# Kernel optimization log

Measured on AMD Instinct MI355X. Metric: run time of the kernel, lower is better.

The kernel has to match this reference:

```python
import jax, jax.numpy as jnp
import numpy as np


def _maxpool2x2(x):
    # x: [N, C, H, W] -> [N, C, H//2, W//2]
    N, C, H, W = x.shape
    x = x.reshape(N, C, H // 2, 2, W // 2, 2)
    return x.max(axis=(3, 5))


def setup_inputs() -> dict:
    key = jax.random.key(0)
    ks = jax.random.split(key, 6)
    N, C, H, W = 16, 64, 64, 64
    x = jax.random.normal(ks[0], (N, C, H, W), dtype=jnp.float32)
    # 1x1 conv weights, stored as [out_ch, in_ch] (kernel is 1x1, no bias)
    w_theta = jax.random.normal(ks[1], (C >> 3, C), dtype=jnp.float32) * 0.05
    w_phi = jax.random.normal(ks[2], (C >> 3, C), dtype=jnp.float32) * 0.05
    w_g = jax.random.normal(ks[3], (C >> 1, C), dtype=jnp.float32) * 0.05
    w_o = jax.random.normal(ks[4], (C, C >> 1), dtype=jnp.float32) * 0.05
    gamma = jax.random.normal(ks[5], (), dtype=jnp.float32)
    return {"x": x, "w_theta": w_theta, "w_phi": w_phi, "w_g": w_g, "w_o": w_o, "gamma": gamma}


def reference(x, w_theta, w_phi, w_g, w_o, gamma):
    N, C, H, W = x.shape
    L = H * W           # location_num
    D = L >> 2          # downsampled_num
    # 1x1 convs as channel contractions
    theta = jnp.einsum('oc,nchw->nohw', w_theta, x).reshape(N, C >> 3, L)
    phi = _maxpool2x2(jnp.einsum('oc,nchw->nohw', w_phi, x)).reshape(N, C >> 3, D)
    attn = jax.nn.softmax(jnp.einsum('nkl,nkd->nld', theta, phi), axis=-1)  # [N, L, D]
    g = _maxpool2x2(jnp.einsum('oc,nchw->nohw', w_g, x)).reshape(N, C >> 1, D)
    attn_g = jnp.einsum('ngd,nld->ngl', g, attn).reshape(N, C >> 1, H, W)
    attn_g = jnp.einsum('og,nghw->nohw', w_o, attn_g)
    return x + gamma * attn_g
```

## Files before the change

### kernel.cpp

```cpp
#include <hip/hip_runtime.h>
#include <hip/hip_bf16.h>
#include <hip/hip_fp16.h>

#define NB 16
#define CCH 64
#define LL 4096
#define DD 1024

typedef _Float16 h8 __attribute__((ext_vector_type(8)));
typedef _Float16 h2 __attribute__((ext_vector_type(2)));
typedef float    f4v __attribute__((ext_vector_type(4)));

#if defined(__has_builtin)
#if __has_builtin(__builtin_amdgcn_fdot2)
#define HAVE_FDOT2 1
#endif
#if __has_builtin(__builtin_amdgcn_exp2f)
#define EXP2F(x) __builtin_amdgcn_exp2f(x)
#endif
#endif
#ifndef EXP2F
#define EXP2F(x) exp2f(x)
#endif

static __device__ __forceinline__ float fdot2f(h2 a, h2 b, float c) {
#ifdef HAVE_FDOT2
    return __builtin_amdgcn_fdot2(a, b, c, false);
#else
    return c + (float)a[0] * (float)b[0] + (float)a[1] * (float)b[1];
#endif
}

#define MFMA16(a, b, c) __builtin_amdgcn_mfma_f32_16x16x32_f16((a), (b), (c), 0, 0, 0)

__global__ __launch_bounds__(256) void prep_kernel(
    const float* __restrict__ x,
    const float* __restrict__ w_theta,
    const float* __restrict__ w_phi,
    const float* __restrict__ w_g,
    _Float16* __restrict__ theta_out,
    _Float16* __restrict__ phi_out,
    _Float16* __restrict__ gT_out)
{
    __shared__ float part[64][193];

    const int n    = blockIdx.x >> 6;
    const int rem  = blockIdx.x & 63;
    const int rg   = rem >> 1;
    const int half = rem & 1;
    const int tid  = threadIdx.x;
    const int cs   = tid >> 6;
    const int pix  = tid & 63;
    const int row  = pix >> 5;
    const int col  = pix & 31;
    const int l    = (rg * 2 + row) * 64 + half * 32 + col;

    const float* xp = x + (size_t)n * CCH * LL + l;
    float xv[16];
#pragma unroll
    for (int c = 0; c < 16; ++c) xv[c] = xp[(size_t)(cs * 16 + c) * LL];

    float f48[48];
#pragma unroll
    for (int k = 0; k < 8; ++k) {
        float a = 0.f;
        const float* w = w_theta + k * 64 + cs * 16;
#pragma unroll
        for (int c = 0; c < 16; ++c) a += w[c] * xv[c];
        f48[k] = a;
    }
#pragma unroll
    for (int k = 0; k < 8; ++k) {
        float a = 0.f;
        const float* w = w_phi + k * 64 + cs * 16;
#pragma unroll
        for (int c = 0; c < 16; ++c) a += w[c] * xv[c];
        f48[8 + k] = a;
    }
#pragma unroll
    for (int j = 0; j < 32; ++j) {
        float a = 0.f;
        const float* w = w_g + j * 64 + cs * 16;
#pragma unroll
        for (int c = 0; c < 16; ++c) a += w[c] * xv[c];
        f48[16 + j] = a;
    }

    {
        float* pp = &part[pix][cs * 48];
#pragma unroll
        for (int f = 0; f < 48; ++f) pp[f] = f48[f];
    }
    __syncthreads();

    float fin[12];
#pragma unroll
    for (int j = 0; j < 12; ++j) {
        int f = cs * 12 + j;
        fin[j] = part[pix][f] + part[pix][48 + f] + part[pix][96 + f] + part[pix][144 + f];
    }

    if (cs == 0) {
        h8 tv;
#pragma unroll
        for (int k = 0; k < 8; ++k) tv[k] = (_Float16)(fin[k] * 1.44269504f);
        *(h8*)(theta_out + ((size_t)n * LL + l) * 8) = tv;
    }

#pragma unroll
    for (int j = 0; j < 12; ++j) part[pix][cs * 12 + j] = fin[j];
    __syncthreads();

    for (int idx = tid; idx < 40 * 16; idx += 256) {
        int f8 = idx >> 4;
        int pc = idx & 15;
        int f  = 8 + f8;
        float v = fmaxf(fmaxf(part[2 * pc][f],      part[2 * pc + 1][f]),
                        fmaxf(part[32 + 2 * pc][f], part[33 + 2 * pc][f]));
        int d = rg * 32 + half * 16 + pc;
        if (f8 < 8) phi_out[((size_t)n * DD + d) * 8 + f8] = (_Float16)v;
        else        gT_out[((size_t)n * 32 + (f8 - 8)) * DD + d] = (_Float16)v;
    }
}

__global__ __launch_bounds__(256, 4) void attn_kernel(
    const float*    __restrict__ x,
    const _Float16* __restrict__ theta,
    const _Float16* __restrict__ phi,
    const _Float16* __restrict__ gT,
    const float*    __restrict__ w_o,
    const float*    __restrict__ gamma_p,
    float*          __restrict__ out)
{
    __shared__ __align__(16) char smem[17152 + 16896 + 512];
    _Float16* phi_s  = (_Float16*)smem;
    float*    out_s  = (float*)smem;
    float*    red    = (float*)(smem + 17152);
    float*    ssum_s = (float*)(smem + 17152 + 16896);

    const int n    = blockIdx.x >> 6;
    const int lblk = blockIdx.x & 63;
    const int tid  = threadIdx.x;
    const int w    = tid >> 6;
    const int g    = w >> 1;
    const int h    = w & 1;
    const int lane = tid & 63;
    const int m16  = lane & 15;
    const int quad = lane >> 4;
    const int l0   = lblk * 64;

    const _Float16* gT_n = gT + (size_t)n * 32 * DD;

    {
        const float4* ps = (const float4*)(phi + (size_t)n * DD * 8);
        float4* pd = (float4*)phi_s;
#pragma unroll
        for (int i = 0; i < 4; ++i) pd[tid + 256 * i] = ps[tid + 256 * i];
    }

    h8 th0 = *(const h8*)(theta + ((size_t)n * LL + l0 + g * 32 + m16) * 8);
    h8 th1 = *(const h8*)(theta + ((size_t)n * LL + l0 + g * 32 + 16 + m16) * 8);
    const h2* t0p = (const h2*)&th0;
    const h2* t1p = (const h2*)&th1;

    h8 wof[4];
#pragma unroll
    for (int v = 0; v < 4; ++v) {
        const float* wr = w_o + (size_t)(m16 + 16 * v) * 32 + quad * 8;
        float4 wa = *(const float4*)wr;
        float4 wb = *(const float4*)(wr + 4);
        wof[v][0] = (_Float16)wa.x; wof[v][1] = (_Float16)wa.y;
        wof[v][2] = (_Float16)wa.z; wof[v][3] = (_Float16)wa.w;
        wof[v][4] = (_Float16)wb.x; wof[v][5] = (_Float16)wb.y;
        wof[v][6] = (_Float16)wb.z; wof[v][7] = (_Float16)wb.w;
    }

    __syncthreads();

    f4v c00 = {0.f, 0.f, 0.f, 0.f}, c01 = c00, c10 = c00, c11 = c00;
    float ssum0 = 0.f, ssum1 = 0.f;

    const _Float16* gr0 = gT_n + (size_t)m16 * DD + h * 512 + quad * 8;
    const _Float16* gr1 = gT_n + (size_t)(16 + m16) * DD + h * 512 + quad * 8;
    const _Float16* pr  = phi_s + (size_t)(h * 512 + quad * 8) * 8;

#pragma unroll 2
    for (int c = 0; c < 16; ++c) {
        const int d0 = c * 32;
        h8 b0 = *(const h8*)(gr0 + d0);
        h8 b1 = *(const h8*)(gr1 + d0);
        h8 a0, a1;
#pragma unroll
        for (int j = 0; j < 8; ++j) {
            h8 ph = *(const h8*)(pr + (size_t)(d0 + j) * 8);
            const h2* pp = (const h2*)&ph;
            float s0 = fdot2f(t0p[0], pp[0], 0.f);
            s0 = fdot2f(t0p[1], pp[1], s0);
            s0 = fdot2f(t0p[2], pp[2], s0);
            s0 = fdot2f(t0p[3], pp[3], s0);
            float s1 = fdot2f(t1p[0], pp[0], 0.f);
            s1 = fdot2f(t1p[1], pp[1], s1);
            s1 = fdot2f(t1p[2], pp[2], s1);
            s1 = fdot2f(t1p[3], pp[3], s1);
            float e0 = EXP2F(s0);
            float e1 = EXP2F(s1);
            ssum0 += e0; ssum1 += e1;
            a0[j] = (_Float16)e0;
            a1[j] = (_Float16)e1;
        }
        c00 = MFMA16(a0, b0, c00);
        c01 = MFMA16(a0, b1, c01);
        c10 = MFMA16(a1, b0, c10);
        c11 = MFMA16(a1, b1, c11);
    }

    ssum0 += __shfl_xor(ssum0, 16); ssum0 += __shfl_xor(ssum0, 32);
    ssum1 += __shfl_xor(ssum1, 16); ssum1 += __shfl_xor(ssum1, 32);

    {
        float* rg = red + (size_t)(g * 2 + h) * 32 * 33;
#pragma unroll
        for (int r = 0; r < 4; ++r) {
            const int rr = quad * 4 + r;
            rg[rr * 33 + m16]             = c00[r];
            rg[rr * 33 + 16 + m16]        = c01[r];
            rg[(16 + rr) * 33 + m16]      = c10[r];
            rg[(16 + rr) * 33 + 16 + m16] = c11[r];
        }
        if (quad == 0) {
            ssum_s[(g * 2 + h) * 32 + m16]      = ssum0;
            ssum_s[(g * 2 + h) * 32 + 16 + m16] = ssum1;
        }
    }
    __syncthreads();

    h8 pa;
    {
        const float* r0 = red + (size_t)(g * 2 + 0) * 32 * 33 + (h * 16 + m16) * 33 + quad * 8;
        const float* r1 = red + (size_t)(g * 2 + 1) * 32 * 33 + (h * 16 + m16) * 33 + quad * 8;
        float ss = ssum_s[(g * 2) * 32 + h * 16 + m16]
                 + ssum_s[(g * 2 + 1) * 32 + h * 16 + m16];
        float inv = 1.0f / ss;
#pragma unroll
        for (int j = 0; j < 8; ++j) pa[j] = (_Float16)((r0[j] + r1[j]) * inv);
    }

    const f4v zero = {0.f, 0.f, 0.f, 0.f};
#pragma unroll
    for (int v = 0; v < 4; ++v) {
        f4v p = MFMA16(pa, wof[v], zero);
        const int och = m16 + 16 * v;
        float* od = out_s + (size_t)och * 67 + g * 32 + h * 16 + quad * 4;
#pragma unroll
        for (int r = 0; r < 4; ++r) od[r] = p[r];
    }
    __syncthreads();

    const float gamma = gamma_p[0];
    const int soch = tid >> 2;
    const int sp   = tid & 3;
    const float* xrow = x   + (size_t)n * CCH * LL + (size_t)soch * LL + l0;
    float*       orow = out + (size_t)n * CCH * LL + (size_t)soch * LL + l0;
    const float* srow = out_s + (size_t)soch * 67;
#pragma unroll
    for (int i = 0; i < 4; ++i) {
        const int q = sp * 16 + i * 4;
        float4 xv = *(const float4*)(xrow + q);
        float4 ov;
        ov.x = xv.x + gamma * srow[q];
        ov.y = xv.y + gamma * srow[q + 1];
        ov.z = xv.z + gamma * srow[q + 2];
        ov.w = xv.w + gamma * srow[q + 3];
        *(float4*)(orow + q) = ov;
    }
}

extern "C" void kernel_launch(void* const* d_in, const int* in_sizes, int n_in,
                              void* d_out, int out_size, void* d_ws, size_t ws_size,
                              hipStream_t stream) {
    const float* x       = (const float*)d_in[0];
    const float* w_theta = (const float*)d_in[1];
    const float* w_phi   = (const float*)d_in[2];
    const float* w_g     = (const float*)d_in[3];
    const float* w_o     = (const float*)d_in[4];
    const float* gamma   = (const float*)d_in[5];
    float* out = (float*)d_out;

    _Float16* theta_h = (_Float16*)d_ws;
    _Float16* phi_h   = theta_h + (size_t)NB * LL * 8;
    _Float16* gT_h    = phi_h   + (size_t)NB * DD * 8;

    prep_kernel<<<1024, 256, 0, stream>>>(x, w_theta, w_phi, w_g,
                                          theta_h, phi_h, gT_h);
    attn_kernel<<<1024, 256, 0, stream>>>(x, theta_h, phi_h, gT_h,
                                          w_o, gamma, out);
}
```

Before: 129.3 us.

## Split attention over 4 D-chunks per block, shuffle-reduce prep features

The attention kernel now gives each block 32 query locations instead of 64 and launches twice as many blocks. Each of the four waves handles a quarter of the 1024 downsampled keys, and the partial results are reduced through LDS. Phi is read straight from global memory instead of being staged in shared memory, and the launch-bounds occupancy hint rises from 4 to 6. In the prep kernel, the cross-channel partial sums and the horizontal max are done with wave shuffles instead of a large LDS buffer and one barrier. This cuts LDS use and synchronisation, at the cost of extra redundant global phi and gT reads and a larger cross-wave reduction.

```diff
diff --git a/kernel.cpp b/kernel.cpp
--- a/kernel.cpp
+++ b/kernel.cpp
@@ -42,88 +42,92 @@
     _Float16* __restrict__ phi_out,
     _Float16* __restrict__ gT_out)
 {
-    __shared__ float part[64][193];
+    __shared__ float pool[2][16][41];
 
     const int n    = blockIdx.x >> 6;
     const int rem  = blockIdx.x & 63;
     const int rg   = rem >> 1;
     const int half = rem & 1;
     const int tid  = threadIdx.x;
-    const int cs   = tid >> 6;
-    const int pix  = tid & 63;
-    const int row  = pix >> 5;
-    const int col  = pix & 31;
-    const int l    = (rg * 2 + row) * 64 + half * 32 + col;
+    const int w    = tid >> 6;
+    const int lane = tid & 63;
+    const int cq   = lane >> 4;
+    const int p    = lane & 15;
+    const int r2   = w >> 1;
+    const int c16  = w & 1;
+    const int row  = rg * 2 + r2;
+    const int col  = half * 32 + c16 * 16 + p;
+    const int l    = row * 64 + col;
 
     const float* xp = x + (size_t)n * CCH * LL + l;
     float xv[16];
 #pragma unroll
-    for (int c = 0; c < 16; ++c) xv[c] = xp[(size_t)(cs * 16 + c) * LL];
+    for (int c = 0; c < 16; ++c) xv[c] = xp[(size_t)(cq * 16 + c) * LL];
 
     float f48[48];
 #pragma unroll
     for (int k = 0; k < 8; ++k) {
         float a = 0.f;
-        const float* w = w_theta + k * 64 + cs * 16;
-#pragma unroll
-        for (int c = 0; c < 16; ++c) a += w[c] * xv[c];
+        const float* wt = w_theta + k * 64 + cq * 16;
+#pragma unroll
+        for (int c = 0; c < 16; ++c) a += wt[c] * xv[c];
         f48[k] = a;
     }
 #pragma unroll
     for (int k = 0; k < 8; ++k) {
         float a = 0.f;
-        const float* w = w_phi + k * 64 + cs * 16;
-#pragma unroll
-        for (int c = 0; c < 16; ++c) a += w[c] * xv[c];
+        const float* wp = w_phi + k * 64 + cq * 16;
+#pragma unroll
+        for (int c = 0; c < 16; ++c) a += wp[c] * xv[c];
         f48[8 + k] = a;
     }
 #pragma unroll
     for (int j = 0; j < 32; ++j) {
         float a = 0.f;
-        const float* w = w_g + j * 64 + cs * 16;
-#pragma unroll
-        for (int c = 0; c < 16; ++c) a += w[c] * xv[c];
+        const float* wg = w_g + j * 64 + cq * 16;
+#pragma unroll
+        for (int c = 0; c < 16; ++c) a += wg[c] * xv[c];
         f48[16 + j] = a;
     }
 
+#pragma unroll
+    for (int f = 0; f < 48; ++f) {
+        f48[f] += __shfl_xor(f48[f], 16);
+        f48[f] += __shfl_xor(f48[f], 32);
+    }
+
+    if (cq == 0) {
+        h8 tv;
+#pragma unroll
+        for (int k = 0; k < 8; ++k) tv[k] = (_Float16)(f48[k] * 1.44269504f);
+        *(h8*)(theta_out + ((size_t)n * LL + l) * 8) = tv;
+    }
+
     {
-        float* pp = &part[pix][cs * 48];
-#pragma unroll
-        for (int f = 0; f < 48; ++f) pp[f] = f48[f];
-    }
-    __syncthreads();
-
-    float fin[12];
-#pragma unroll
-    for (int j = 0; j < 12; ++j) {
-        int f = cs * 12 + j;
-        fin[j] = part[pix][f] + part[pix][48 + f] + part[pix][96 + f] + part[pix][144 + f];
-    }
-
-    if (cs == 0) {
-        h8 tv;
-#pragma unroll
-        for (int k = 0; k < 8; ++k) tv[k] = (_Float16)(fin[k] * 1.44269504f);
-        *(h8*)(theta_out + ((size_t)n * LL + l) * 8) = tv;
-    }
-
-#pragma unroll
-    for (int j = 0; j < 12; ++j) part[pix][cs * 12 + j] = fin[j];
-    __syncthreads();
-
-    for (int idx = tid; idx < 40 * 16; idx += 256) {
-        int f8 = idx >> 4;
-        int pc = idx & 15;
-        int f  = 8 + f8;
-        float v = fmaxf(fmaxf(part[2 * pc][f],      part[2 * pc + 1][f]),
-                        fmaxf(part[32 + 2 * pc][f], part[33 + 2 * pc][f]));
-        int d = rg * 32 + half * 16 + pc;
+        const int cp = c16 * 8 + (p >> 1);
+#pragma unroll
+        for (int j = 0; j < 12; ++j) {
+            const int f = cq * 12 + j;
+            float v = f48[f];
+            float hmax = fmaxf(v, __shfl_xor(v, 1));
+            if (f >= 8 && (p & 1) == 0)
+                pool[r2][cp][f - 8] = hmax;
+        }
+    }
+    __syncthreads();
+
+    const int d_base = rg * 32 + half * 16;
+    for (int idx = tid; idx < 640; idx += 256) {
+        const int f8 = idx >> 4;
+        const int pc = idx & 15;
+        float v = fmaxf(pool[0][pc][f8], pool[1][pc][f8]);
+        const int d = d_base + pc;
         if (f8 < 8) phi_out[((size_t)n * DD + d) * 8 + f8] = (_Float16)v;
         else        gT_out[((size_t)n * 32 + (f8 - 8)) * DD + d] = (_Float16)v;
     }
 }
 
-__global__ __launch_bounds__(256, 4) void attn_kernel(
+__global__ __launch_bounds__(256, 6) void attn_kernel(
     const float*    __restrict__ x,
     const _Float16* __restrict__ theta,
     const _Float16* __restrict__ phi,
@@ -132,60 +136,50 @@
     const float*    __restrict__ gamma_p,
     float*          __restrict__ out)
 {
-    __shared__ __align__(16) char smem[17152 + 16896 + 512];
-    _Float16* phi_s  = (_Float16*)smem;
-    float*    out_s  = (float*)smem;
-    float*    red    = (float*)(smem + 17152);
-    float*    ssum_s = (float*)(smem + 17152 + 16896);
-
-    const int n    = blockIdx.x >> 6;
-    const int lblk = blockIdx.x & 63;
+    __shared__ __align__(16) char smem[16896 + 512];
+    float* red    = (float*)smem;
+    float* ssum_s = (float*)(smem + 16896);
+    float* out_s  = (float*)smem;
+
+    const int n    = blockIdx.x >> 7;
+    const int lblk = blockIdx.x & 127;
     const int tid  = threadIdx.x;
-    const int w    = tid >> 6;
-    const int g    = w >> 1;
-    const int h    = w & 1;
+    const int h    = tid >> 6;
     const int lane = tid & 63;
     const int m16  = lane & 15;
     const int quad = lane >> 4;
-    const int l0   = lblk * 64;
-
-    const _Float16* gT_n = gT + (size_t)n * 32 * DD;
-
-    {
-        const float4* ps = (const float4*)(phi + (size_t)n * DD * 8);
-        float4* pd = (float4*)phi_s;
-#pragma unroll
-        for (int i = 0; i < 4; ++i) pd[tid + 256 * i] = ps[tid + 256 * i];
-    }
-
-    h8 th0 = *(const h8*)(theta + ((size_t)n * LL + l0 + g * 32 + m16) * 8);
-    h8 th1 = *(const h8*)(theta + ((size_t)n * LL + l0 + g * 32 + 16 + m16) * 8);
+    const int l0   = lblk * 32;
+
+    const _Float16* gT_n  = gT  + (size_t)n * 32 * DD;
+    const _Float16* phi_n = phi + (size_t)n * DD * 8;
+
+    h8 th0 = *(const h8*)(theta + ((size_t)n * LL + l0 + m16) * 8);
+    h8 th1 = *(const h8*)(theta + ((size_t)n * LL + l0 + 16 + m16) * 8);
     const h2* t0p = (const h2*)&th0;
     const h2* t1p = (const h2*)&th1;
 
-    h8 wof[4];
-#pragma unroll
-    for (int v = 0; v < 4; ++v) {
-        const float* wr = w_o + (size_t)(m16 + 16 * v) * 32 + quad * 8;
+    const int vp = h >> 1;
+    h8 wof[2];
+#pragma unroll
+    for (int i = 0; i < 2; ++i) {
+        const float* wr = w_o + (size_t)(m16 + 16 * (vp * 2 + i)) * 32 + quad * 8;
         float4 wa = *(const float4*)wr;
         float4 wb = *(const float4*)(wr + 4);
-        wof[v][0] = (_Float16)wa.x; wof[v][1] = (_Float16)wa.y;
-        wof[v][2] = (_Float16)wa.z; wof[v][3] = (_Float16)wa.w;
-        wof[v][4] = (_Float16)wb.x; wof[v][5] = (_Float16)wb.y;
-        wof[v][6] = (_Float16)wb.z; wof[v][7] = (_Float16)wb.w;
-    }
-
-    __syncthreads();
+        wof[i][0] = (_Float16)wa.x; wof[i][1] = (_Float16)wa.y;
+        wof[i][2] = (_Float16)wa.z; wof[i][3] = (_Float16)wa.w;
+        wof[i][4] = (_Float16)wb.x; wof[i][5] = (_Float16)wb.y;
+        wof[i][6] = (_Float16)wb.z; wof[i][7] = (_Float16)wb.w;
+    }
 
     f4v c00 = {0.f, 0.f, 0.f, 0.f}, c01 = c00, c10 = c00, c11 = c00;
     float ssum0 = 0.f, ssum1 = 0.f;
 
-    const _Float16* gr0 = gT_n + (size_t)m16 * DD + h * 512 + quad * 8;
-    const _Float16* gr1 = gT_n + (size_t)(16 + m16) * DD + h * 512 + quad * 8;
-    const _Float16* pr  = phi_s + (size_t)(h * 512 + quad * 8) * 8;
+    const _Float16* gr0 = gT_n + (size_t)m16 * DD + h * 256 + quad * 8;
+    const _Float16* gr1 = gT_n + (size_t)(16 + m16) * DD + h * 256 + quad * 8;
+    const _Float16* pr  = phi_n + (size_t)(h * 256 + quad * 8) * 8;
 
 #pragma unroll 2
-    for (int c = 0; c < 16; ++c) {
+    for (int c = 0; c < 8; ++c) {
         const int d0 = c * 32;
         h8 b0 = *(const h8*)(gr0 + d0);
         h8 b1 = *(const h8*)(gr1 + d0);
@@ -218,7 +212,7 @@
     ssum1 += __shfl_xor(ssum1, 16); ssum1 += __shfl_xor(ssum1, 32);
 
     {
-        float* rg = red + (size_t)(g * 2 + h) * 32 * 33;
+        float* rg = red + (size_t)h * 32 * 33;
 #pragma unroll
         for (int r = 0; r < 4; ++r) {
             const int rr = quad * 4 + r;
@@ -228,50 +222,53 @@
             rg[(16 + rr) * 33 + 16 + m16] = c11[r];
         }
         if (quad == 0) {
-            ssum_s[(g * 2 + h) * 32 + m16]      = ssum0;
-            ssum_s[(g * 2 + h) * 32 + 16 + m16] = ssum1;
-        }
-    }
-    __syncthreads();
-
+            ssum_s[h * 32 + m16]      = ssum0;
+            ssum_s[h * 32 + 16 + m16] = ssum1;
+        }
+    }
+    __syncthreads();
+
+    const int t = h & 1;
     h8 pa;
     {
-        const float* r0 = red + (size_t)(g * 2 + 0) * 32 * 33 + (h * 16 + m16) * 33 + quad * 8;
-        const float* r1 = red + (size_t)(g * 2 + 1) * 32 * 33 + (h * 16 + m16) * 33 + quad * 8;
-        float ss = ssum_s[(g * 2) * 32 + h * 16 + m16]
-                 + ssum_s[(g * 2 + 1) * 32 + h * 16 + m16];
+        const int q = t * 16 + m16;
+        const float* rq = red + q * 33 + quad * 8;
+        float ss = ssum_s[q] + ssum_s[32 + q] + ssum_s[64 + q] + ssum_s[96 + q];
         float inv = 1.0f / ss;
 #pragma unroll
-        for (int j = 0; j < 8; ++j) pa[j] = (_Float16)((r0[j] + r1[j]) * inv);
-    }
+        for (int j = 0; j < 8; ++j) {
+            float sv = rq[j] + rq[32 * 33 + j] + rq[64 * 33 + j] + rq[96 * 33 + j];
+            pa[j] = (_Float16)(sv * inv);
+        }
+    }
+    __syncthreads();
 
     const f4v zero = {0.f, 0.f, 0.f, 0.f};
 #pragma unroll
-    for (int v = 0; v < 4; ++v) {
-        f4v p = MFMA16(pa, wof[v], zero);
-        const int och = m16 + 16 * v;
-        float* od = out_s + (size_t)och * 67 + g * 32 + h * 16 + quad * 4;
-#pragma unroll
-        for (int r = 0; r < 4; ++r) od[r] = p[r];
+    for (int i = 0; i < 2; ++i) {
+        f4v pv = MFMA16(pa, wof[i], zero);
+        const int och = m16 + 16 * (vp * 2 + i);
+        float* od = out_s + (size_t)och * 33 + t * 16 + quad * 4;
+#pragma unroll
+        for (int r = 0; r < 4; ++r) od[r] = pv[r];
     }
     __syncthreads();
 
     const float gamma = gamma_p[0];
     const int soch = tid >> 2;
-    const int sp   = tid & 3;
-    const float* xrow = x   + (size_t)n * CCH * LL + (size_t)soch * LL + l0;
-    float*       orow = out + (size_t)n * CCH * LL + (size_t)soch * LL + l0;
-    const float* srow = out_s + (size_t)soch * 67;
-#pragma unroll
-    for (int i = 0; i < 4; ++i) {
-        const int q = sp * 16 + i * 4;
-        float4 xv = *(const float4*)(xrow + q);
+    const int qoff = (tid & 3) * 8;
+    const float* xrow = x   + (size_t)n * CCH * LL + (size_t)soch * LL + l0 + qoff;
+    float*       orow = out + (size_t)n * CCH * LL + (size_t)soch * LL + l0 + qoff;
+    const float* srow = out_s + (size_t)soch * 33 + qoff;
+#pragma unroll
+    for (int i = 0; i < 2; ++i) {
+        float4 xv = *(const float4*)(xrow + i * 4);
         float4 ov;
-        ov.x = xv.x + gamma * srow[q];
-        ov.y = xv.y + gamma * srow[q + 1];
-        ov.z = xv.z + gamma * srow[q + 2];
-        ov.w = xv.w + gamma * srow[q + 3];
-        *(float4*)(orow + q) = ov;
+        ov.x = xv.x + gamma * srow[i * 4];
+        ov.y = xv.y + gamma * srow[i * 4 + 1];
+        ov.z = xv.z + gamma * srow[i * 4 + 2];
+        ov.w = xv.w + gamma * srow[i * 4 + 3];
+        *(float4*)(orow + i * 4) = ov;
     }
 }
 
@@ -292,6 +289,6 @@
 
     prep_kernel<<<1024, 256, 0, stream>>>(x, w_theta, w_phi, w_g,
                                           theta_h, phi_h, gT_h);
-    attn_kernel<<<1024, 256, 0, stream>>>(x, theta_h, phi_h, gT_h,
+    attn_kernel<<<2048, 256, 0, stream>>>(x, theta_h, phi_h, gT_h,
                                           w_o, gamma, out);
 }
```

After: 166.2 us. 28.5% more time.

## Halve attention tile to 32 locations and split D across four waves

Applied to the files above, without the earlier changes.

The attention kernel now handles 32 query locations per block instead of 64, with each of the four waves covering a quarter of the D dimension, and the grid doubles to 2048 blocks. Shared memory is cut by aliasing the partial-sum buffer with the phi buffer, and launch bounds rise to 6 blocks per CU to raise occupancy. The trade-off is that each block reloads phi and gT for half the locations, doubling that redundant traffic, and adds extra barriers plus a four-way cross-wave reduction.

```diff
diff --git a/kernel.cpp b/kernel.cpp
--- a/kernel.cpp
+++ b/kernel.cpp
@@ -123,7 +123,7 @@
     }
 }
 
-__global__ __launch_bounds__(256, 4) void attn_kernel(
+__global__ __launch_bounds__(256, 6) void attn_kernel(
     const float*    __restrict__ x,
     const _Float16* __restrict__ theta,
     const _Float16* __restrict__ phi,
@@ -132,22 +132,20 @@
     const float*    __restrict__ gamma_p,
     float*          __restrict__ out)
 {
-    __shared__ __align__(16) char smem[17152 + 16896 + 512];
+    __shared__ __align__(16) char smem[18944 + 512];
     _Float16* phi_s  = (_Float16*)smem;
+    float*    red    = (float*)smem;
     float*    out_s  = (float*)smem;
-    float*    red    = (float*)(smem + 17152);
-    float*    ssum_s = (float*)(smem + 17152 + 16896);
-
-    const int n    = blockIdx.x >> 6;
-    const int lblk = blockIdx.x & 63;
+    float*    ssum_s = (float*)(smem + 18944);
+
+    const int n    = blockIdx.x >> 7;
+    const int lblk = blockIdx.x & 127;
     const int tid  = threadIdx.x;
-    const int w    = tid >> 6;
-    const int g    = w >> 1;
-    const int h    = w & 1;
+    const int h    = tid >> 6;
     const int lane = tid & 63;
     const int m16  = lane & 15;
     const int quad = lane >> 4;
-    const int l0   = lblk * 64;
+    const int l0   = lblk * 32;
 
     const _Float16* gT_n = gT + (size_t)n * 32 * DD;
 
@@ -158,21 +156,22 @@
         for (int i = 0; i < 4; ++i) pd[tid + 256 * i] = ps[tid + 256 * i];
     }
 
-    h8 th0 = *(const h8*)(theta + ((size_t)n * LL + l0 + g * 32 + m16) * 8);
-    h8 th1 = *(const h8*)(theta + ((size_t)n * LL + l0 + g * 32 + 16 + m16) * 8);
+    h8 th0 = *(const h8*)(theta + ((size_t)n * LL + l0 + m16) * 8);
+    h8 th1 = *(const h8*)(theta + ((size_t)n * LL + l0 + 16 + m16) * 8);
     const h2* t0p = (const h2*)&th0;
     const h2* t1p = (const h2*)&th1;
 
-    h8 wof[4];
-#pragma unroll
-    for (int v = 0; v < 4; ++v) {
-        const float* wr = w_o + (size_t)(m16 + 16 * v) * 32 + quad * 8;
+    const int vp = h >> 1;
+    h8 wof[2];
+#pragma unroll
+    for (int i = 0; i < 2; ++i) {
+        const float* wr = w_o + (size_t)(m16 + 16 * (vp * 2 + i)) * 32 + quad * 8;
         float4 wa = *(const float4*)wr;
         float4 wb = *(const float4*)(wr + 4);
-        wof[v][0] = (_Float16)wa.x; wof[v][1] = (_Float16)wa.y;
-        wof[v][2] = (_Float16)wa.z; wof[v][3] = (_Float16)wa.w;
-        wof[v][4] = (_Float16)wb.x; wof[v][5] = (_Float16)wb.y;
-        wof[v][6] = (_Float16)wb.z; wof[v][7] = (_Float16)wb.w;
+        wof[i][0] = (_Float16)wa.x; wof[i][1] = (_Float16)wa.y;
+        wof[i][2] = (_Float16)wa.z; wof[i][3] = (_Float16)wa.w;
+        wof[i][4] = (_Float16)wb.x; wof[i][5] = (_Float16)wb.y;
+        wof[i][6] = (_Float16)wb.z; wof[i][7] = (_Float16)wb.w;
     }
 
     __syncthreads();
@@ -180,12 +179,12 @@
     f4v c00 = {0.f, 0.f, 0.f, 0.f}, c01 = c00, c10 = c00, c11 = c00;
     float ssum0 = 0.f, ssum1 = 0.f;
 
-    const _Float16* gr0 = gT_n + (size_t)m16 * DD + h * 512 + quad * 8;
-    const _Float16* gr1 = gT_n + (size_t)(16 + m16) * DD + h * 512 + quad * 8;
-    const _Float16* pr  = phi_s + (size_t)(h * 512 + quad * 8) * 8;
+    const _Float16* gr0 = gT_n + (size_t)m16 * DD + h * 256 + quad * 8;
+    const _Float16* gr1 = gT_n + (size_t)(16 + m16) * DD + h * 256 + quad * 8;
+    const _Float16* pr  = phi_s + (size_t)(h * 256 + quad * 8) * 8;
 
 #pragma unroll 2
-    for (int c = 0; c < 16; ++c) {
+    for (int c = 0; c < 8; ++c) {
         const int d0 = c * 32;
         h8 b0 = *(const h8*)(gr0 + d0);
         h8 b1 = *(const h8*)(gr1 + d0);
@@ -216,62 +215,65 @@
 
     ssum0 += __shfl_xor(ssum0, 16); ssum0 += __shfl_xor(ssum0, 32);
     ssum1 += __shfl_xor(ssum1, 16); ssum1 += __shfl_xor(ssum1, 32);
-
-    {
-        float* rg = red + (size_t)(g * 2 + h) * 32 * 33;
+    if (quad == 0) {
+        ssum_s[h * 32 + m16]      = ssum0;
+        ssum_s[h * 32 + 16 + m16] = ssum1;
+    }
+    __syncthreads();
+
+    {
+        float* rg = red + (size_t)h * 32 * 37;
 #pragma unroll
         for (int r = 0; r < 4; ++r) {
             const int rr = quad * 4 + r;
-            rg[rr * 33 + m16]             = c00[r];
-            rg[rr * 33 + 16 + m16]        = c01[r];
-            rg[(16 + rr) * 33 + m16]      = c10[r];
-            rg[(16 + rr) * 33 + 16 + m16] = c11[r];
+            rg[rr * 37 + m16]             = c00[r];
+            rg[rr * 37 + 16 + m16]        = c01[r];
+            rg[(16 + rr) * 37 + m16]      = c10[r];
+            rg[(16 + rr) * 37 + 16 + m16] = c11[r];
         }
-        if (quad == 0) {
-            ssum_s[(g * 2 + h) * 32 + m16]      = ssum0;
-            ssum_s[(g * 2 + h) * 32 + 16 + m16] = ssum1;
+    }
+    __syncthreads();
+
+    const int t = h & 1;
+    h8 pa;
+    {
+        const int q = t * 16 + m16;
+        const float* rq = red + q * 37 + quad * 8;
+        float ss = ssum_s[q] + ssum_s[32 + q] + ssum_s[64 + q] + ssum_s[96 + q];
+        float inv = 1.0f / ss;
+#pragma unroll
+        for (int j = 0; j < 8; ++j) {
+            float sv = rq[j] + rq[32 * 37 + j] + rq[64 * 37 + j] + rq[96 * 37 + j];
+            pa[j] = (_Float16)(sv * inv);
         }
     }
     __syncthreads();
 
-    h8 pa;
-    {
-        const float* r0 = red + (size_t)(g * 2 + 0) * 32 * 33 + (h * 16 + m16) * 33 + quad * 8;
-        const float* r1 = red + (size_t)(g * 2 + 1) * 32 * 33 + (h * 16 + m16) * 33 + quad * 8;
-        float ss = ssum_s[(g * 2) * 32 + h * 16 + m16]
-                 + ssum_s[(g * 2 + 1) * 32 + h * 16 + m16];
-        float inv = 1.0f / ss;
-#pragma unroll
-        for (int j = 0; j < 8; ++j) pa[j] = (_Float16)((r0[j] + r1[j]) * inv);
-    }
-
     const f4v zero = {0.f, 0.f, 0.f, 0.f};
 #pragma unroll
-    for (int v = 0; v < 4; ++v) {
-        f4v p = MFMA16(pa, wof[v], zero);
-        const int och = m16 + 16 * v;
-        float* od = out_s + (size_t)och * 67 + g * 32 + h * 16 + quad * 4;
-#pragma unroll
-        for (int r = 0; r < 4; ++r) od[r] = p[r];
+    for (int i = 0; i < 2; ++i) {
+        f4v pv = MFMA16(pa, wof[i], zero);
+        const int och = m16 + 16 * (vp * 2 + i);
+        float* od = out_s + (size_t)(t * 16 + quad * 4) * 68 + och;
+#pragma unroll
+        for (int r = 0; r < 4; ++r) od[r * 68] = pv[r];
     }
     __syncthreads();
 
     const float gamma = gamma_p[0];
     const int soch = tid >> 2;
-    const int sp   = tid & 3;
-    const float* xrow = x   + (size_t)n * CCH * LL + (size_t)soch * LL + l0;
-    float*       orow = out + (size_t)n * CCH * LL + (size_t)soch * LL + l0;
-    const float* srow = out_s + (size_t)soch * 67;
-#pragma unroll
-    for (int i = 0; i < 4; ++i) {
-        const int q = sp * 16 + i * 4;
-        float4 xv = *(const float4*)(xrow + q);
+    const int qoff = (tid & 3) * 8;
+    const float* xrow = x   + (size_t)n * CCH * LL + (size_t)soch * LL + l0 + qoff;
+    float*       orow = out + (size_t)n * CCH * LL + (size_t)soch * LL + l0 + qoff;
+#pragma unroll
+    for (int i = 0; i < 2; ++i) {
+        float4 xv = *(const float4*)(xrow + i * 4);
         float4 ov;
-        ov.x = xv.x + gamma * srow[q];
-        ov.y = xv.y + gamma * srow[q + 1];
-        ov.z = xv.z + gamma * srow[q + 2];
-        ov.w = xv.w + gamma * srow[q + 3];
-        *(float4*)(orow + q) = ov;
+        ov.x = xv.x + gamma * out_s[(qoff + i * 4)     * 68 + soch];
+        ov.y = xv.y + gamma * out_s[(qoff + i * 4 + 1) * 68 + soch];
+        ov.z = xv.z + gamma * out_s[(qoff + i * 4 + 2) * 68 + soch];
+        ov.w = xv.w + gamma * out_s[(qoff + i * 4 + 3) * 68 + soch];
+        *(float4*)(orow + i * 4) = ov;
     }
 }
 
@@ -292,6 +294,6 @@
 
     prep_kernel<<<1024, 256, 0, stream>>>(x, w_theta, w_phi, w_g,
                                           theta_h, phi_h, gT_h);
-    attn_kernel<<<1024, 256, 0, stream>>>(x, theta_h, phi_h, gT_h,
+    attn_kernel<<<2048, 256, 0, stream>>>(x, theta_h, phi_h, gT_h,
                                           w_o, gamma, out);
 }
```

Result: no change. 131.5 us (+1.7%).
